# Kernel tuning notes

Measured on AMD Instinct MI355X. Metric: run time of the kernel, lower is better.

Reference implementation:

```python
import jax, jax.numpy as jnp
import numpy as np

IN_DIM, OUT_DIM = 256, 128
N_NODES, N_EDGES = 50000, 800000


def _glorot(key, shape):
    fan_in = shape[-1]
    return jax.random.normal(key, shape, dtype=jnp.float32) / jnp.sqrt(jnp.float32(fan_in))


def setup_inputs() -> dict:
    key = jax.random.key(0)
    ks = jax.random.split(key, 16)
    features1 = jax.random.normal(ks[0], (N_NODES, IN_DIM), dtype=jnp.float32)
    edge_index = jax.random.randint(ks[1], (2, N_EDGES), 0, N_NODES, dtype=jnp.int32)
    return {
        "features1": features1,
        "edge_index": edge_index,
        # encoder conv1: in->out
        "Wl_e1": _glorot(ks[2], (OUT_DIM, IN_DIM)), "bl_e1": jnp.zeros((OUT_DIM,), jnp.float32), "Wr_e1": _glorot(ks[3], (OUT_DIM, IN_DIM)),
        # encoder conv2: out->out
        "Wl_e2": _glorot(ks[4], (OUT_DIM, OUT_DIM)), "bl_e2": jnp.zeros((OUT_DIM,), jnp.float32), "Wr_e2": _glorot(ks[5], (OUT_DIM, OUT_DIM)),
        # fc: out->out
        "W_fc": _glorot(ks[6], (OUT_DIM, OUT_DIM)), "b_fc": jnp.zeros((OUT_DIM,), jnp.float32),
        # decoder conv1: out->out
        "Wl_d1": _glorot(ks[7], (OUT_DIM, OUT_DIM)), "bl_d1": jnp.zeros((OUT_DIM,), jnp.float32), "Wr_d1": _glorot(ks[8], (OUT_DIM, OUT_DIM)),
        # decoder conv2: out->in
        "Wl_d2": _glorot(ks[9], (IN_DIM, OUT_DIM)), "bl_d2": jnp.zeros((IN_DIM,), jnp.float32), "Wr_d2": _glorot(ks[10], (IN_DIM, OUT_DIM)),
    }


def _sage_conv(x, src, dst, inv_deg, Wl, bl, Wr):
    # mean aggregation of neighbor messages x[src] at destination nodes
    agg = jax.ops.segment_sum(x[src], dst, num_segments=N_NODES) * inv_deg  # [N, d_in]
    out = agg @ Wl.T + bl + x @ Wr.T  # lin_l(agg) + lin_r(x)
    # F.normalize(out, p=2, dim=-1)
    nrm = jnp.maximum(jnp.linalg.norm(out, axis=-1, keepdims=True), 1e-12)
    return out / nrm


def reference(features1, edge_index, Wl_e1, bl_e1, Wr_e1, Wl_e2, bl_e2, Wr_e2,
              W_fc, b_fc, Wl_d1, bl_d1, Wr_d1, Wl_d2, bl_d2, Wr_d2):
    src, dst = edge_index[0], edge_index[1]
    deg = jax.ops.segment_sum(jnp.ones((src.shape[0],), jnp.float32), dst, num_segments=N_NODES)
    inv_deg = (1.0 / jnp.maximum(deg, 1.0))[:, None]
    # encoder
    h = _sage_conv(features1, src, dst, inv_deg, Wl_e1, bl_e1, Wr_e1)
    x1 = _sage_conv(h, src, dst, inv_deg, Wl_e2, bl_e2, Wr_e2)
    # bottleneck linear
    x = x1 @ W_fc.T + b_fc
    # decoder
    h = _sage_conv(x, src, dst, inv_deg, Wl_d1, bl_d1, Wr_d1)
    x1_rec = _sage_conv(h, src, dst, inv_deg, Wl_d2, bl_d2, Wr_d2)
    return (x1, x1_rec)
```

## Files before the change

kernel.cpp:

```cpp
#include <hip/hip_runtime.h>
#include <hip/hip_bf16.h>
#include <math.h>

#define N_NODES 50000
#define N_EDGES 800000
#define SLOT_CAP 64
#define NB128 391
#define FILLB 1024

typedef short s16x8 __attribute__((ext_vector_type(8)));
typedef float f32x4 __attribute__((ext_vector_type(4)));

static __device__ __forceinline__ unsigned short f2bf(float x) {
    __hip_bfloat16 b = __float2bfloat16(x);
    return *(unsigned short*)&b;
}
static __device__ __forceinline__ float2 bfu2f2(unsigned int u) {
    __hip_bfloat162 b = *(__hip_bfloat162*)&u;
    return __bfloat1622float2(b);
}
static __device__ __forceinline__ unsigned int packbf2(float x, float y) {
    return (unsigned int)f2bf(x) | ((unsigned int)f2bf(y) << 16);
}

#define FEATN (N_NODES * 256)
#define O_WL_E1 (FEATN)
#define O_WR_E1 (FEATN + 32768)
#define O_WL_E2 (FEATN + 65536)
#define O_WR_E2 (FEATN + 81920)
#define O_D2    (FEATN + 98304)
#define PREP_TOT (FEATN + 163840)
#define O_WD1C  (FEATN + 163840)
#define POOL_TOT (FEATN + 196608)

__global__ __launch_bounds__(256) void k_prep(const float* __restrict__ feat,
                                              const float* __restrict__ wle1, const float* __restrict__ wre1,
                                              const float* __restrict__ wle2, const float* __restrict__ wre2,
                                              const float* __restrict__ wld2, const float* __restrict__ wrd2,
                                              unsigned short* __restrict__ dstp) {
    const int tot4 = PREP_TOT / 4;
    for (int i = blockIdx.x * blockDim.x + threadIdx.x; i < tot4; i += gridDim.x * blockDim.x) {
        int e = i * 4;
        const float* s;
        int off;
        if      (e < O_WL_E1) { s = feat; off = e; }
        else if (e < O_WR_E1) { s = wle1; off = e - O_WL_E1; }
        else if (e < O_WL_E2) { s = wre1; off = e - O_WR_E1; }
        else if (e < O_WR_E2) { s = wle2; off = e - O_WL_E2; }
        else if (e < O_D2)    { s = wre2; off = e - O_WR_E2; }
        else {
            int rel = e - O_D2;
            int row = rel >> 8, half = (rel >> 7) & 1, col = rel & 127;
            s = half ? wrd2 : wld2;
            off = row * 128 + col;
        }
        float4 v = *(const float4*)&s[off];
        ushort4 u;
        u.x = f2bf(v.x); u.y = f2bf(v.y); u.z = f2bf(v.z); u.w = f2bf(v.w);
        *(ushort4*)&dstp[e] = u;
    }
}

__global__ __launch_bounds__(128) void k_compose(const float* __restrict__ wld1,
                                                 const float* __restrict__ wrd1,
                                                 const float* __restrict__ wfc,
                                                 const float* __restrict__ bfc,
                                                 const float* __restrict__ bld1,
                                                 unsigned short* __restrict__ outw,
                                                 float* __restrict__ bT, float* __restrict__ bP) {
    const float* WX = blockIdx.y ? wrd1 : wld1;
    if (blockIdx.x < 128) {
        int r = blockIdx.x, c = threadIdx.x;
        float acc = 0.0f;
        for (int j = 0; j < 128; j++) acc += WX[r * 128 + j] * wfc[j * 128 + c];
        outw[blockIdx.y * 16384 + r * 128 + c] = f2bf(acc);
    } else {
        int t = threadIdx.x;
        float acc = 0.0f;
        for (int j = 0; j < 128; j++) acc += WX[t * 128 + j] * bfc[j];
        if (blockIdx.y == 0) bT[t] = acc;
        else                 bP[t] = acc + bld1[t];
    }
}

template <int K>
static __device__ __forceinline__ void gemm_body(int bxm, int by,
                                                 const unsigned short* __restrict__ X,
                                                 const unsigned short* __restrict__ W,
                                                 const float* __restrict__ bias0,
                                                 const float* __restrict__ bias1,
                                                 unsigned short* __restrict__ Y,
                                                 int N, int Ystride) {
    constexpr int CH = K / 8;
    __shared__ unsigned short Ws[128 * K];
    const unsigned short* Wsrc = W + (size_t)by * 128 * K;
    for (int idx = threadIdx.x; idx < 128 * CH; idx += 256) {
        int n = idx / CH, c = idx % CH;
        uint4 v = *(const uint4*)&Wsrc[n * K + c * 8];
        int cs = c ^ (n & 15);
        *(uint4*)&Ws[n * K + cs * 8] = v;
    }
    __syncthreads();

    const int wid = threadIdx.x >> 6, lane = threadIdx.x & 63;
    const int row0 = bxm * 128 + wid * 32;
    const int lrow = lane & 15;
    const int lk8  = lane >> 4;
    f32x4 acc[2][8] = {};

    s16x8 a_cur[2];
#pragma unroll
    for (int i = 0; i < 2; i++) {
        int r = row0 + i * 16 + lrow;
        s16x8 av = {};
        if (r < N) av = *(const s16x8*)&X[(size_t)r * K + lk8 * 8];
        a_cur[i] = av;
    }

#pragma unroll
    for (int ks = 0; ks < K; ks += 32) {
        s16x8 a_nxt[2] = {};
        if (ks + 32 < K) {
#pragma unroll
            for (int i = 0; i < 2; i++) {
                int r = row0 + i * 16 + lrow;
                if (r < N) a_nxt[i] = *(const s16x8*)&X[(size_t)r * K + ks + 32 + lk8 * 8];
            }
        }
#pragma unroll
        for (int nf = 0; nf < 8; nf++) {
            int n = nf * 16 + lrow;
            int c = (ks >> 3) + lk8;
            int cs = c ^ (n & 15);
            s16x8 b = *(const s16x8*)&Ws[n * K + cs * 8];
            acc[0][nf] = __builtin_amdgcn_mfma_f32_16x16x32_bf16(a_cur[0], b, acc[0][nf], 0, 0, 0);
            acc[1][nf] = __builtin_amdgcn_mfma_f32_16x16x32_bf16(a_cur[1], b, acc[1][nf], 0, 0, 0);
        }
        a_cur[0] = a_nxt[0];
        a_cur[1] = a_nxt[1];
    }

    const float* bias = (by == 0) ? bias0 : bias1;
    const int ccol = lane & 15, crow0 = (lane >> 4) * 4;
    const int ycol0 = by * 128;
#pragma unroll
    for (int nf = 0; nf < 8; nf++) {
        int lcol = nf * 16 + ccol;
        float bv = bias ? bias[lcol] : 0.0f;
#pragma unroll
        for (int i = 0; i < 2; i++) {
#pragma unroll
            for (int j = 0; j < 4; j++) {
                int grow = row0 + i * 16 + crow0 + j;
                if (grow < N) Y[(size_t)grow * Ystride + ycol0 + lcol] = f2bf(acc[i][nf][j] + bv);
            }
        }
    }
}

template <int K>
__global__ __launch_bounds__(256) void k_gmm2(const unsigned short* __restrict__ X,
                                              const unsigned short* __restrict__ W,
                                              const float* __restrict__ bias0,
                                              const float* __restrict__ bias1,
                                              unsigned short* __restrict__ Y,
                                              int N, int Ystride) {
    gemm_body<K>(blockIdx.x, blockIdx.y, X, W, bias0, bias1, Y, N, Ystride);
}

__global__ __launch_bounds__(256) void k_g1f(const unsigned short* __restrict__ X,
                                             const unsigned short* __restrict__ W,
                                             const float* __restrict__ bias1,
                                             unsigned short* __restrict__ Y,
                                             const int* __restrict__ esrc,
                                             const int* __restrict__ edst,
                                             int* __restrict__ cnt,
                                             int* __restrict__ slots) {
    if (blockIdx.x < 2 * NB128) {
        gemm_body<256>(blockIdx.x >> 1, blockIdx.x & 1, X, W, nullptr, bias1, Y, N_NODES, 256);
    } else {
        const int fb = blockIdx.x - 2 * NB128;
        for (int e = fb * 256 + threadIdx.x; e < N_EDGES; e += FILLB * 256) {
            int d = edst[e];
            int pos = atomicAdd(&cnt[d], 1);
            if (pos < SLOT_CAP) slots[d * SLOT_CAP + pos] = esrc[e];
        }
    }
}

__global__ __launch_bounds__(256) void k_gmmn(const unsigned short* __restrict__ X,
                                              const unsigned short* __restrict__ W,
                                              const float* __restrict__ bias,
                                              float* __restrict__ OUT, int N) {
    __shared__ unsigned short Ws[128 * 256];
    const int wid = threadIdx.x >> 6, lane = threadIdx.x & 63;
    const int row0 = blockIdx.x * 128 + wid * 32;
    const int lrow = lane & 15;
    const int lk8  = lane >> 4;
    const int ccol = lane & 15, crow0 = (lane >> 4) * 4;
    f32x4 acc[2][2][8] = {};

#pragma unroll
    for (int half = 0; half < 2; half++) {
        __syncthreads();
        const unsigned short* Wsrc = W + (size_t)half * 128 * 256;
        for (int idx = threadIdx.x; idx < 128 * 32; idx += 256) {
            int n = idx / 32, c = idx % 32;
            uint4 v = *(const uint4*)&Wsrc[n * 256 + c * 8];
            int cs = c ^ (n & 15);
            *(uint4*)&Ws[n * 256 + cs * 8] = v;
        }
        __syncthreads();

        s16x8 a_cur[2];
#pragma unroll
        for (int i = 0; i < 2; i++) {
            int r = row0 + i * 16 + lrow;
            s16x8 av = {};
            if (r < N) av = *(const s16x8*)&X[(size_t)r * 256 + lk8 * 8];
            a_cur[i] = av;
        }
#pragma unroll
        for (int ks = 0; ks < 256; ks += 32) {
            s16x8 a_nxt[2] = {};
            if (ks + 32 < 256) {
#pragma unroll
                for (int i = 0; i < 2; i++) {
                    int r = row0 + i * 16 + lrow;
                    if (r < N) a_nxt[i] = *(const s16x8*)&X[(size_t)r * 256 + ks + 32 + lk8 * 8];
                }
            }
#pragma unroll
            for (int nf = 0; nf < 8; nf++) {
                int n = nf * 16 + lrow;
                int c = (ks >> 3) + lk8;
                int cs = c ^ (n & 15);
                s16x8 b = *(const s16x8*)&Ws[n * 256 + cs * 8];
                acc[half][0][nf] = __builtin_amdgcn_mfma_f32_16x16x32_bf16(a_cur[0], b, acc[half][0][nf], 0, 0, 0);
                acc[half][1][nf] = __builtin_amdgcn_mfma_f32_16x16x32_bf16(a_cur[1], b, acc[half][1][nf], 0, 0, 0);
            }
            a_cur[0] = a_nxt[0];
            a_cur[1] = a_nxt[1];
        }
    }

#pragma unroll
    for (int half = 0; half < 2; half++)
#pragma unroll
        for (int nf = 0; nf < 8; nf++) {
            float bv = bias[half * 128 + nf * 16 + ccol];
#pragma unroll
            for (int i = 0; i < 2; i++)
#pragma unroll
                for (int j = 0; j < 4; j++) acc[half][i][nf][j] += bv;
        }
    float rs[2][4];
#pragma unroll
    for (int i = 0; i < 2; i++)
#pragma unroll
        for (int j = 0; j < 4; j++) {
            float ss = 0.0f;
#pragma unroll
            for (int half = 0; half < 2; half++)
#pragma unroll
                for (int nf = 0; nf < 8; nf++) ss += acc[half][i][nf][j] * acc[half][i][nf][j];
            ss += __shfl_xor(ss, 1); ss += __shfl_xor(ss, 2);
            ss += __shfl_xor(ss, 4); ss += __shfl_xor(ss, 8);
            rs[i][j] = 1.0f / fmaxf(sqrtf(ss), 1e-12f);
        }
#pragma unroll
    for (int i = 0; i < 2; i++)
#pragma unroll
        for (int j = 0; j < 4; j++) {
            int grow = row0 + i * 16 + crow0 + j;
            if (grow < N) {
                float r = rs[i][j];
#pragma unroll
                for (int half = 0; half < 2; half++)
#pragma unroll
                    for (int nf = 0; nf < 8; nf++)
                        OUT[(size_t)grow * 256 + half * 128 + nf * 16 + ccol] = acc[half][i][nf][j] * r;
            }
        }
}

template <bool WRITE_F32>
__global__ __launch_bounds__(256) void k_aggfin4(const uint4* __restrict__ TP,
                                                 const int* __restrict__ slots,
                                                 const int* __restrict__ cnt,
                                                 float* __restrict__ OUTF,
                                                 uint4* __restrict__ OUTB,
                                                 int ostride4, int ooff4) {
    const int wave = (blockIdx.x * blockDim.x + threadIdx.x) >> 6;
    const int lane = threadIdx.x & 63;
    if (wave >= N_NODES) return;
    const int q = lane & 15, sub = lane >> 4;
    int deg = cnt[wave];
    deg = min(deg, SLOT_CAP);
    const int base = wave * SLOT_CAP;
    float acc[8] = {};
    int i = sub * 4;
    for (; i + 3 < deg; i += 16) {
        int4 nb = *(const int4*)&slots[base + i];
        uint4 v0 = TP[(size_t)nb.x * 32 + q];
        uint4 v1 = TP[(size_t)nb.y * 32 + q];
        uint4 v2 = TP[(size_t)nb.z * 32 + q];
        uint4 v3 = TP[(size_t)nb.w * 32 + q];
        float2 a0 = bfu2f2(v0.x), a1 = bfu2f2(v0.y), a2 = bfu2f2(v0.z), a3 = bfu2f2(v0.w);
        float2 b0 = bfu2f2(v1.x), b1 = bfu2f2(v1.y), b2 = bfu2f2(v1.z), b3 = bfu2f2(v1.w);
        float2 c0 = bfu2f2(v2.x), c1 = bfu2f2(v2.y), c2 = bfu2f2(v2.z), c3 = bfu2f2(v2.w);
        float2 d0 = bfu2f2(v3.x), d1 = bfu2f2(v3.y), d2 = bfu2f2(v3.z), d3 = bfu2f2(v3.w);
        acc[0] += (a0.x + b0.x) + (c0.x + d0.x); acc[1] += (a0.y + b0.y) + (c0.y + d0.y);
        acc[2] += (a1.x + b1.x) + (c1.x + d1.x); acc[3] += (a1.y + b1.y) + (c1.y + d1.y);
        acc[4] += (a2.x + b2.x) + (c2.x + d2.x); acc[5] += (a2.y + b2.y) + (c2.y + d2.y);
        acc[6] += (a3.x + b3.x) + (c3.x + d3.x); acc[7] += (a3.y + b3.y) + (c3.y + d3.y);
    }
    const int r0 = deg & ~3;
    if (sub == ((r0 >> 2) & 3)) {
        for (int j = r0; j < deg; j++) {
            uint4 v = TP[(size_t)slots[base + j] * 32 + q];
            float2 a0 = bfu2f2(v.x), a1 = bfu2f2(v.y), a2 = bfu2f2(v.z), a3 = bfu2f2(v.w);
            acc[0] += a0.x; acc[1] += a0.y; acc[2] += a1.x; acc[3] += a1.y;
            acc[4] += a2.x; acc[5] += a2.y; acc[6] += a3.x; acc[7] += a3.y;
        }
    }
#pragma unroll
    for (int k = 0; k < 8; k++) {
        acc[k] += __shfl_xor(acc[k], 16);
        acc[k] += __shfl_xor(acc[k], 32);
    }
    const float inv = 1.0f / fmaxf((float)deg, 1.0f);
    uint4 pv = TP[(size_t)wave * 32 + 16 + q];
    float2 p0 = bfu2f2(pv.x), p1 = bfu2f2(pv.y), p2 = bfu2f2(pv.z), p3 = bfu2f2(pv.w);
    float o[8];
    o[0] = p0.x + inv * acc[0]; o[1] = p0.y + inv * acc[1];
    o[2] = p1.x + inv * acc[2]; o[3] = p1.y + inv * acc[3];
    o[4] = p2.x + inv * acc[4]; o[5] = p2.y + inv * acc[5];
    o[6] = p3.x + inv * acc[6]; o[7] = p3.y + inv * acc[7];
    float ss = 0.0f;
#pragma unroll
    for (int k = 0; k < 8; k++) ss += o[k] * o[k];
    ss += __shfl_xor(ss, 1); ss += __shfl_xor(ss, 2);
    ss += __shfl_xor(ss, 4); ss += __shfl_xor(ss, 8);
    float r = 1.0f / fmaxf(sqrtf(ss), 1e-12f);
#pragma unroll
    for (int k = 0; k < 8; k++) o[k] *= r;
    if (lane < 16) {
        if constexpr (WRITE_F32) {
            ((float4*)OUTF)[(size_t)wave * 32 + q * 2]     = make_float4(o[0], o[1], o[2], o[3]);
            ((float4*)OUTF)[(size_t)wave * 32 + q * 2 + 1] = make_float4(o[4], o[5], o[6], o[7]);
        }
        uint4 u;
        u.x = packbf2(o[0], o[1]); u.y = packbf2(o[2], o[3]);
        u.z = packbf2(o[4], o[5]); u.w = packbf2(o[6], o[7]);
        OUTB[(size_t)wave * ostride4 + ooff4 + q] = u;
    }
}

__global__ __launch_bounds__(256) void k_agg4(const uint4* __restrict__ IN,
                                              const int* __restrict__ slots,
                                              const int* __restrict__ cnt,
                                              uint4* __restrict__ OUT,
                                              int istride4, int ioff4, int ostride4, int ooff4) {
    const int wave = (blockIdx.x * blockDim.x + threadIdx.x) >> 6;
    const int lane = threadIdx.x & 63;
    if (wave >= N_NODES) return;
    const int q = lane & 15, sub = lane >> 4;
    int deg = cnt[wave];
    deg = min(deg, SLOT_CAP);
    const int base = wave * SLOT_CAP;
    float acc[8] = {};
    int i = sub * 4;
    for (; i + 3 < deg; i += 16) {
        int4 nb = *(const int4*)&slots[base + i];
        uint4 v0 = IN[(size_t)nb.x * istride4 + ioff4 + q];
        uint4 v1 = IN[(size_t)nb.y * istride4 + ioff4 + q];
        uint4 v2 = IN[(size_t)nb.z * istride4 + ioff4 + q];
        uint4 v3 = IN[(size_t)nb.w * istride4 + ioff4 + q];
        float2 a0 = bfu2f2(v0.x), a1 = bfu2f2(v0.y), a2 = bfu2f2(v0.z), a3 = bfu2f2(v0.w);
        float2 b0 = bfu2f2(v1.x), b1 = bfu2f2(v1.y), b2 = bfu2f2(v1.z), b3 = bfu2f2(v1.w);
        float2 c0 = bfu2f2(v2.x), c1 = bfu2f2(v2.y), c2 = bfu2f2(v2.z), c3 = bfu2f2(v2.w);
        float2 d0 = bfu2f2(v3.x), d1 = bfu2f2(v3.y), d2 = bfu2f2(v3.z), d3 = bfu2f2(v3.w);
        acc[0] += (a0.x + b0.x) + (c0.x + d0.x); acc[1] += (a0.y + b0.y) + (c0.y + d0.y);
        acc[2] += (a1.x + b1.x) + (c1.x + d1.x); acc[3] += (a1.y + b1.y) + (c1.y + d1.y);
        acc[4] += (a2.x + b2.x) + (c2.x + d2.x); acc[5] += (a2.y + b2.y) + (c2.y + d2.y);
        acc[6] += (a3.x + b3.x) + (c3.x + d3.x); acc[7] += (a3.y + b3.y) + (c3.y + d3.y);
    }
    const int r0 = deg & ~3;
    if (sub == ((r0 >> 2) & 3)) {
        for (int j = r0; j < deg; j++) {
            uint4 v = IN[(size_t)slots[base + j] * istride4 + ioff4 + q];
            float2 a0 = bfu2f2(v.x), a1 = bfu2f2(v.y), a2 = bfu2f2(v.z), a3 = bfu2f2(v.w);
            acc[0] += a0.x; acc[1] += a0.y; acc[2] += a1.x; acc[3] += a1.y;
            acc[4] += a2.x; acc[5] += a2.y; acc[6] += a3.x; acc[7] += a3.y;
        }
    }
#pragma unroll
    for (int k = 0; k < 8; k++) {
        acc[k] += __shfl_xor(acc[k], 16);
        acc[k] += __shfl_xor(acc[k], 32);
    }
    const float inv = 1.0f / fmaxf((float)deg, 1.0f);
    if (lane < 16) {
        uint4 u;
        u.x = packbf2(inv * acc[0], inv * acc[1]);
        u.y = packbf2(inv * acc[2], inv * acc[3]);
        u.z = packbf2(inv * acc[4], inv * acc[5]);
        u.w = packbf2(inv * acc[6], inv * acc[7]);
        OUT[(size_t)wave * ostride4 + ooff4 + q] = u;
    }
}

extern "C" void kernel_launch(void* const* d_in, const int* in_sizes, int n_in,
                              void* d_out, int out_size, void* d_ws, size_t ws_size,
                              hipStream_t stream) {
    const float* feat  = (const float*)d_in[0];
    const int*   ei    = (const int*)d_in[1];
    const int*   src   = ei;
    const int*   dst   = ei + N_EDGES;
    const float* Wl_e1 = (const float*)d_in[2];
    const float* bl_e1 = (const float*)d_in[3];
    const float* Wr_e1 = (const float*)d_in[4];
    const float* Wl_e2 = (const float*)d_in[5];
    const float* bl_e2 = (const float*)d_in[6];
    const float* Wr_e2 = (const float*)d_in[7];
    const float* W_fc  = (const float*)d_in[8];
    const float* b_fc  = (const float*)d_in[9];
    const float* Wl_d1 = (const float*)d_in[10];
    const float* bl_d1 = (const float*)d_in[11];
    const float* Wr_d1 = (const float*)d_in[12];
    const float* Wl_d2 = (const float*)d_in[13];
    const float* bl_d2 = (const float*)d_in[14];
    const float* Wr_d2 = (const float*)d_in[15];

    char* w = (char*)d_ws;
    auto alloc = [&](size_t bytes) -> void* {
        void* p = (void*)w;
        w += (bytes + 255) & ~(size_t)255;
        return p;
    };
    int* cnt   = (int*)alloc((size_t)N_NODES * 4);
    int* slots = (int*)alloc((size_t)N_NODES * SLOT_CAP * 4);
    unsigned short* bfpool = (unsigned short*)alloc((size_t)POOL_TOT * 2);
    unsigned short* TP   = (unsigned short*)alloc((size_t)N_NODES * 256 * 2);
    unsigned short* hb   = (unsigned short*)alloc((size_t)N_NODES * 128 * 2);
    unsigned short* x1b  = (unsigned short*)alloc((size_t)N_NODES * 128 * 2);
    unsigned short* X2   = (unsigned short*)alloc((size_t)N_NODES * 256 * 2);
    float* bT = (float*)alloc(128 * 4);
    float* bP = (float*)alloc(128 * 4);

    unsigned short* featb = bfpool;
    float* x1     = (float*)d_out;
    float* x1_rec = (float*)d_out + (size_t)N_NODES * 128;

    hipMemsetAsync(cnt, 0, (size_t)N_NODES * 4, stream);

    k_compose<<<dim3(129, 2), 128, 0, stream>>>(Wl_d1, Wr_d1, W_fc, b_fc, bl_d1,
                                                bfpool + O_WD1C, bT, bP);
    k_prep<<<2048, 256, 0, stream>>>(feat, Wl_e1, Wr_e1, Wl_e2, Wr_e2, Wl_d2, Wr_d2, bfpool);

    const int WPB = (N_NODES * 64 + 255) / 256;

    k_g1f<<<2 * NB128 + FILLB, 256, 0, stream>>>(featb, bfpool + O_WL_E1, bl_e1, TP,
                                                 src, dst, cnt, slots);
    k_aggfin4<false><<<WPB, 256, 0, stream>>>((const uint4*)TP, slots, cnt, nullptr, (uint4*)hb, 16, 0);
    k_gmm2<128><<<dim3(NB128, 2), 256, 0, stream>>>(hb, bfpool + O_WL_E2, nullptr, bl_e2, TP, N_NODES, 256);
    k_aggfin4<true><<<WPB, 256, 0, stream>>>((const uint4*)TP, slots, cnt, x1, (uint4*)x1b, 16, 0);
    k_gmm2<128><<<dim3(NB128, 2), 256, 0, stream>>>(x1b, bfpool + O_WD1C, bT, bP, TP, N_NODES, 256);
    k_aggfin4<false><<<WPB, 256, 0, stream>>>((const uint4*)TP, slots, cnt, nullptr, (uint4*)X2, 32, 16);
    k_agg4<<<WPB, 256, 0, stream>>>((const uint4*)X2, slots, cnt, (uint4*)X2, 32, 16, 32, 0);
    k_gmmn<<<NB128, 256, 0, stream>>>(X2, bfpool + O_D2, bl_d2, x1_rec, N_NODES);
}
```

Baseline: 328.6 us.

## Fuse prep, compose and half of edge fill into one kernel; halve GEMM LDS

Merges the bf16 conversion kernel and the weight-composition kernel into a single launch, and moves the first half of the edge-slot fill into that launch, leaving the second half in the first GEMM kernel. The GEMM body now stages weights in LDS in 128-wide K chunks instead of all of K at once, which halves shared memory for K=256 and may raise occupancy, at the cost of an extra barrier and a reload step. These changes aim to cut launch count and overlap the atomic fill with the memory-bound conversion. The risk is that the atomic fill work now contends with the conversion traffic.

```diff
diff --git a/kernel.cpp b/kernel.cpp
--- a/kernel.cpp
+++ b/kernel.cpp
@@ -6,7 +6,10 @@
 #define N_EDGES 800000
 #define SLOT_CAP 64
 #define NB128 391
-#define FILLB 1024
+#define PREPB 2048
+#define FILLA 512
+#define FILLB 512
+#define E_SPLIT 400000
 
 typedef short s16x8 __attribute__((ext_vector_type(8)));
 typedef float f32x4 __attribute__((ext_vector_type(4)));
@@ -33,53 +36,64 @@
 #define O_WD1C  (FEATN + 163840)
 #define POOL_TOT (FEATN + 196608)
 
-__global__ __launch_bounds__(256) void k_prep(const float* __restrict__ feat,
-                                              const float* __restrict__ wle1, const float* __restrict__ wre1,
-                                              const float* __restrict__ wle2, const float* __restrict__ wre2,
-                                              const float* __restrict__ wld2, const float* __restrict__ wrd2,
-                                              unsigned short* __restrict__ dstp) {
-    const int tot4 = PREP_TOT / 4;
-    for (int i = blockIdx.x * blockDim.x + threadIdx.x; i < tot4; i += gridDim.x * blockDim.x) {
-        int e = i * 4;
-        const float* s;
-        int off;
-        if      (e < O_WL_E1) { s = feat; off = e; }
-        else if (e < O_WR_E1) { s = wle1; off = e - O_WL_E1; }
-        else if (e < O_WL_E2) { s = wre1; off = e - O_WR_E1; }
-        else if (e < O_WR_E2) { s = wle2; off = e - O_WL_E2; }
-        else if (e < O_D2)    { s = wre2; off = e - O_WR_E2; }
-        else {
-            int rel = e - O_D2;
-            int row = rel >> 8, half = (rel >> 7) & 1, col = rel & 127;
-            s = half ? wrd2 : wld2;
-            off = row * 128 + col;
-        }
-        float4 v = *(const float4*)&s[off];
-        ushort4 u;
-        u.x = f2bf(v.x); u.y = f2bf(v.y); u.z = f2bf(v.z); u.w = f2bf(v.w);
-        *(ushort4*)&dstp[e] = u;
-    }
-}
-
-__global__ __launch_bounds__(128) void k_compose(const float* __restrict__ wld1,
-                                                 const float* __restrict__ wrd1,
-                                                 const float* __restrict__ wfc,
-                                                 const float* __restrict__ bfc,
-                                                 const float* __restrict__ bld1,
-                                                 unsigned short* __restrict__ outw,
-                                                 float* __restrict__ bT, float* __restrict__ bP) {
-    const float* WX = blockIdx.y ? wrd1 : wld1;
-    if (blockIdx.x < 128) {
-        int r = blockIdx.x, c = threadIdx.x;
-        float acc = 0.0f;
-        for (int j = 0; j < 128; j++) acc += WX[r * 128 + j] * wfc[j * 128 + c];
-        outw[blockIdx.y * 16384 + r * 128 + c] = f2bf(acc);
+__global__ __launch_bounds__(256) void k_pfc(const float* __restrict__ feat,
+                                             const float* __restrict__ wle1, const float* __restrict__ wre1,
+                                             const float* __restrict__ wle2, const float* __restrict__ wre2,
+                                             const float* __restrict__ wld2, const float* __restrict__ wrd2,
+                                             const float* __restrict__ wld1, const float* __restrict__ wrd1,
+                                             const float* __restrict__ wfc,  const float* __restrict__ bfc,
+                                             const float* __restrict__ bld1,
+                                             unsigned short* __restrict__ dstp,
+                                             const int* __restrict__ esrc, const int* __restrict__ edst,
+                                             int* __restrict__ cnt, int* __restrict__ slots,
+                                             float* __restrict__ bT, float* __restrict__ bP) {
+    if (blockIdx.x < PREPB) {
+        const int tot4 = PREP_TOT / 4;
+        for (int i = blockIdx.x * blockDim.x + threadIdx.x; i < tot4; i += PREPB * 256) {
+            int e = i * 4;
+            const float* s;
+            int off;
+            if      (e < O_WL_E1) { s = feat; off = e; }
+            else if (e < O_WR_E1) { s = wle1; off = e - O_WL_E1; }
+            else if (e < O_WL_E2) { s = wre1; off = e - O_WR_E1; }
+            else if (e < O_WR_E2) { s = wle2; off = e - O_WL_E2; }
+            else if (e < O_D2)    { s = wre2; off = e - O_WR_E2; }
+            else {
+                int rel = e - O_D2;
+                int row = rel >> 8, half = (rel >> 7) & 1, col = rel & 127;
+                s = half ? wrd2 : wld2;
+                off = row * 128 + col;
+            }
+            float4 v = *(const float4*)&s[off];
+            ushort4 u;
+            u.x = f2bf(v.x); u.y = f2bf(v.y); u.z = f2bf(v.z); u.w = f2bf(v.w);
+            *(ushort4*)&dstp[e] = u;
+        }
+    } else if (blockIdx.x < PREPB + FILLA) {
+        const int fb = blockIdx.x - PREPB;
+        for (int e = fb * 256 + threadIdx.x; e < E_SPLIT; e += FILLA * 256) {
+            int d = edst[e];
+            int pos = atomicAdd(&cnt[d], 1);
+            if (pos < SLOT_CAP) slots[d * SLOT_CAP + pos] = esrc[e];
+        }
     } else {
-        int t = threadIdx.x;
-        float acc = 0.0f;
-        for (int j = 0; j < 128; j++) acc += WX[t * 128 + j] * bfc[j];
-        if (blockIdx.y == 0) bT[t] = acc;
-        else                 bP[t] = acc + bld1[t];
+        const int cid = blockIdx.x - PREPB - FILLA;
+        const int byy = cid / 129;
+        const int bxx = cid % 129;
+        const float* WX = byy ? wrd1 : wld1;
+        const int t = threadIdx.x;
+        if (t < 128) {
+            if (bxx < 128) {
+                float acc = 0.0f;
+                for (int j = 0; j < 128; j++) acc += WX[bxx * 128 + j] * wfc[j * 128 + t];
+                ((unsigned short*)dstp)[O_WD1C + byy * 16384 + bxx * 128 + t] = f2bf(acc);
+            } else {
+                float acc = 0.0f;
+                for (int j = 0; j < 128; j++) acc += WX[t * 128 + j] * bfc[j];
+                if (byy == 0) bT[t] = acc;
+                else          bP[t] = acc + bld1[t];
+            }
+        }
     }
 }
 
@@ -91,53 +105,56 @@
                                                  const float* __restrict__ bias1,
                                                  unsigned short* __restrict__ Y,
                                                  int N, int Ystride) {
-    constexpr int CH = K / 8;
-    __shared__ unsigned short Ws[128 * K];
+    __shared__ unsigned short Ws[128 * 128];
     const unsigned short* Wsrc = W + (size_t)by * 128 * K;
-    for (int idx = threadIdx.x; idx < 128 * CH; idx += 256) {
-        int n = idx / CH, c = idx % CH;
-        uint4 v = *(const uint4*)&Wsrc[n * K + c * 8];
-        int cs = c ^ (n & 15);
-        *(uint4*)&Ws[n * K + cs * 8] = v;
-    }
-    __syncthreads();
-
     const int wid = threadIdx.x >> 6, lane = threadIdx.x & 63;
     const int row0 = bxm * 128 + wid * 32;
     const int lrow = lane & 15;
     const int lk8  = lane >> 4;
     f32x4 acc[2][8] = {};
 
-    s16x8 a_cur[2];
-#pragma unroll
-    for (int i = 0; i < 2; i++) {
-        int r = row0 + i * 16 + lrow;
-        s16x8 av = {};
-        if (r < N) av = *(const s16x8*)&X[(size_t)r * K + lk8 * 8];
-        a_cur[i] = av;
-    }
-
-#pragma unroll
-    for (int ks = 0; ks < K; ks += 32) {
-        s16x8 a_nxt[2] = {};
-        if (ks + 32 < K) {
-#pragma unroll
-            for (int i = 0; i < 2; i++) {
-                int r = row0 + i * 16 + lrow;
-                if (r < N) a_nxt[i] = *(const s16x8*)&X[(size_t)r * K + ks + 32 + lk8 * 8];
-            }
-        }
-#pragma unroll
-        for (int nf = 0; nf < 8; nf++) {
-            int n = nf * 16 + lrow;
-            int c = (ks >> 3) + lk8;
+#pragma unroll
+    for (int half = 0; half < K / 128; half++) {
+        if (half) __syncthreads();
+        for (int idx = threadIdx.x; idx < 128 * 16; idx += 256) {
+            int n = idx / 16, c = idx % 16;
+            uint4 v = *(const uint4*)&Wsrc[n * K + half * 128 + c * 8];
             int cs = c ^ (n & 15);
-            s16x8 b = *(const s16x8*)&Ws[n * K + cs * 8];
-            acc[0][nf] = __builtin_amdgcn_mfma_f32_16x16x32_bf16(a_cur[0], b, acc[0][nf], 0, 0, 0);
-            acc[1][nf] = __builtin_amdgcn_mfma_f32_16x16x32_bf16(a_cur[1], b, acc[1][nf], 0, 0, 0);
-        }
-        a_cur[0] = a_nxt[0];
-        a_cur[1] = a_nxt[1];
+            *(uint4*)&Ws[n * 128 + cs * 8] = v;
+        }
+        __syncthreads();
+
+        const int kbase = half * 128;
+        s16x8 a_cur[2];
+#pragma unroll
+        for (int i = 0; i < 2; i++) {
+            int r = row0 + i * 16 + lrow;
+            s16x8 av = {};
+            if (r < N) av = *(const s16x8*)&X[(size_t)r * K + kbase + lk8 * 8];
+            a_cur[i] = av;
+        }
+#pragma unroll
+        for (int ks = 0; ks < 128; ks += 32) {
+            s16x8 a_nxt[2] = {};
+            if (ks + 32 < 128) {
+#pragma unroll
+                for (int i = 0; i < 2; i++) {
+                    int r = row0 + i * 16 + lrow;
+                    if (r < N) a_nxt[i] = *(const s16x8*)&X[(size_t)r * K + kbase + ks + 32 + lk8 * 8];
+                }
+            }
+#pragma unroll
+            for (int nf = 0; nf < 8; nf++) {
+                int n = nf * 16 + lrow;
+                int c = (ks >> 3) + lk8;
+                int cs = c ^ (n & 15);
+                s16x8 b = *(const s16x8*)&Ws[n * 128 + cs * 8];
+                acc[0][nf] = __builtin_amdgcn_mfma_f32_16x16x32_bf16(a_cur[0], b, acc[0][nf], 0, 0, 0);
+                acc[1][nf] = __builtin_amdgcn_mfma_f32_16x16x32_bf16(a_cur[1], b, acc[1][nf], 0, 0, 0);
+            }
+            a_cur[0] = a_nxt[0];
+            a_cur[1] = a_nxt[1];
+        }
     }
 
     const float* bias = (by == 0) ? bias0 : bias1;
@@ -180,7 +197,7 @@
         gemm_body<256>(blockIdx.x >> 1, blockIdx.x & 1, X, W, nullptr, bias1, Y, N_NODES, 256);
     } else {
         const int fb = blockIdx.x - 2 * NB128;
-        for (int e = fb * 256 + threadIdx.x; e < N_EDGES; e += FILLB * 256) {
+        for (int e = E_SPLIT + fb * 256 + threadIdx.x; e < N_EDGES; e += FILLB * 256) {
             int d = edst[e];
             int pos = atomicAdd(&cnt[d], 1);
             if (pos < SLOT_CAP) slots[d * SLOT_CAP + pos] = esrc[e];
@@ -455,9 +472,10 @@
 
     hipMemsetAsync(cnt, 0, (size_t)N_NODES * 4, stream);
 
-    k_compose<<<dim3(129, 2), 128, 0, stream>>>(Wl_d1, Wr_d1, W_fc, b_fc, bl_d1,
-                                                bfpool + O_WD1C, bT, bP);
-    k_prep<<<2048, 256, 0, stream>>>(feat, Wl_e1, Wr_e1, Wl_e2, Wr_e2, Wl_d2, Wr_d2, bfpool);
+    k_pfc<<<PREPB + FILLA + 258, 256, 0, stream>>>(
+        feat, Wl_e1, Wr_e1, Wl_e2, Wr_e2, Wl_d2, Wr_d2,
+        Wl_d1, Wr_d1, W_fc, b_fc, bl_d1,
+        bfpool, src, dst, cnt, slots, bT, bP);
 
     const int WPB = (N_NODES * 64 + 255) / 256;
 
```

After: 320.3 us. 1.03x faster.
